# Kernel optimization log

Measured on AMD Instinct MI355X. Metric: run time of the kernel, lower is better.

The kernel has to match this reference:

```python
import jax, jax.numpy as jnp
import numpy as np

BEAM = 10; MAX_LEN = 32; PAD = 1; BOS = 2; EOS = 3
NEG = jnp.float32(-1e30)


def lstm_cell(x, h, c, Wih, Whh, bih, bhh):
    # PyTorch LSTMCell gate order: i, f, g, o
    gates = x @ Wih.T + bih + h @ Whh.T + bhh
    i, f, g, o = jnp.split(gates, 4, axis=-1)
    c2 = jax.nn.sigmoid(f) * c + jax.nn.sigmoid(i) * jnp.tanh(g)
    h2 = jax.nn.sigmoid(o) * jnp.tanh(c2)
    return h2, c2


def setup_inputs() -> dict:
    key = jax.random.key(0)
    ks = jax.random.split(key, 14)
    G, P, E, H, S = 1000, 50000, 500, 500, 32
    s = lambda k, shape: jax.random.normal(k, shape, jnp.float32) * 0.05
    return {
        "g_seq": jax.random.randint(ks[0], (S, 1), 0, G),
        "enc_emb": s(ks[1], (G, E)),
        "enc_Wih": s(ks[2], (4 * H, E)), "enc_Whh": s(ks[3], (4 * H, H)),
        "enc_bih": s(ks[4], (4 * H,)), "enc_bhh": s(ks[5], (4 * H,)),
        "dec_emb": s(ks[6], (P, E)),
        "dec_Wih": s(ks[7], (4 * H, E)), "dec_Whh": s(ks[8], (4 * H, H)),
        "dec_bih": s(ks[9], (4 * H,)), "dec_bhh": s(ks[10], (4 * H,)),
        "attn_W": s(ks[11], (H, 2 * H)),
        "out_W": s(ks[12], (P, H)),
        "out_b": s(ks[13], (P,)),
    }


def reference(g_seq, enc_emb, enc_Wih, enc_Whh, enc_bih, enc_bhh,
              dec_emb, dec_Wih, dec_Whh, dec_bih, dec_bhh,
              attn_W, out_W, out_b):
    S = g_seq.shape[0]
    H = enc_Whh.shape[1]
    P = out_W.shape[0]

    # ---- encoder: unidirectional LSTMCell over seq, batch = 1 ----
    e_seq = enc_emb[g_seq[:, 0]]  # (S, E)
    def enc_step(carry, e):
        h, c = carry
        h, c = lstm_cell(e[None, :], h, c, enc_Wih, enc_Whh, enc_bih, enc_bhh)
        return (h, c), h[0]
    h0 = jnp.zeros((1, H), jnp.float32)
    (h, c), outs = jax.lax.scan(enc_step, (h0, h0), e_seq)  # outs: (S, H)

    # expand encoder state / context to beam
    context = jnp.broadcast_to(outs[None, :, :], (BEAM, S, H))
    h = jnp.broadcast_to(h, (BEAM, H))
    c = jnp.broadcast_to(c, (BEAM, H))
    scores = jnp.zeros((BEAM,), jnp.float32)
    tokens = jnp.full((BEAM,), PAD, jnp.int32).at[0].set(BOS)
    row0 = (jnp.arange(BEAM)[:, None] == 0)  # first-step mask: only beam 0 valid

    # ---- beam-search decode loop (run full max_len; early-eos break omitted,
    #      see notes: with eos=3 it only changes output when eos tops beam 0) ----
    def dec_step(carry, t):
        h, c, scores, tokens = carry
        e = dec_emb[tokens]                                   # (BEAM, E)
        h2, c2 = lstm_cell(e, h, c, dec_Wih, dec_Whh, dec_bih, dec_bhh)
        # dot attention
        attn = jax.nn.softmax(jnp.einsum('bsh,bh->bs', context, h2), axis=1)
        wctx = jnp.einsum('bs,bsh->bh', attn, context)
        o = jnp.tanh(jnp.concatenate([h2, wctx], axis=1) @ attn_W.T)
        logp = jax.nn.log_softmax(o @ out_W.T + out_b, axis=1)  # (BEAM, P)
        # first step: only beam 0 participates (original uses workd_lk[0])
        beam_lk = jnp.where(t == 0,
                            jnp.where(row0, logp, NEG),
                            logp + scores[:, None])
        best, idx = jax.lax.top_k(beam_lk.reshape(-1), BEAM)
        prev_k = idx // P
        next_y = idx - prev_k * P
        return (h2[prev_k], c2[prev_k], best, next_y), (prev_k, next_y)

    (_, _, scores, _), (prevKs, nextYs) = jax.lax.scan(
        dec_step, (h, c, scores, tokens), jnp.arange(MAX_LEN))

    # ---- hypothesis traceback, vectorized over beams ----
    def tb_step(k, t):
        tok = nextYs[t][k]
        return prevKs[t][k], tok
    _, toks = jax.lax.scan(tb_step, jnp.arange(BEAM), jnp.arange(MAX_LEN - 1, -1, -1))
    hyps = toks[::-1].T  # (BEAM, MAX_LEN)
    return hyps
```

## Files before the change

### kernel.cpp

```cpp
#include <hip/hip_runtime.h>
#include <math.h>

#define BEAM   10
#define MAXLEN 32
#define SLEN   32
#define HD     500
#define ED     500
#define G4     2000
#define PV     50000
#define NEGF   (-1e30f)

#define OFF_X      0
#define OFF_CBUF   64000
#define OFF_GBUF   65000
#define OFF_CTX    69000
#define OFF_DH     85000
#define OFF_DC     90000
#define OFF_DG     95000
#define OFF_H2     115000
#define OFF_C2     120000
#define OFF_O      130000
#define OFF_SCD    135000
#define OFF_TOK    135020
#define OFF_PREVK  135040
#define OFF_NEXTY  135360
#define OFF_PARTD  136000
#define OFF_CAND   152000
#define OFF_LOG    160000
#define OFF_OWT    660000
#define NEED_T_BYTES ((size_t)(OFF_OWT + (size_t)HD * PV) * 4)

typedef unsigned long long u64;

__device__ __forceinline__ float sigf(float x) { return 1.f / (1.f + expf(-x)); }

__device__ __forceinline__ unsigned fkey(float f) {
    unsigned u = __float_as_uint(f);
    return (u & 0x80000000u) ? ~u : (u | 0x80000000u);
}
__device__ __forceinline__ float unfkey(unsigned k) {
    unsigned u = (k & 0x80000000u) ? (k & 0x7fffffffu) : ~k;
    return __uint_as_float(u);
}

__global__ void k_prep(const int* __restrict__ g_seq, const float* __restrict__ enc_emb,
                       const float* __restrict__ Wih, const float* __restrict__ bih,
                       const float* __restrict__ bhh, float* __restrict__ X,
                       float* __restrict__ cbuf0) {
    if (blockIdx.x == 0) {
        for (int j = threadIdx.x; j < HD; j += 256) cbuf0[j] = 0.f;
    }
    int wv = (blockIdx.x * blockDim.x + threadIdx.x) >> 6;
    int lane = threadIdx.x & 63;
    if (wv >= SLEN * G4) return;
    int t = wv / G4, r = wv - t * G4;
    const float* emb = enc_emb + (size_t)g_seq[t] * ED;
    const float* w = Wih + (size_t)r * ED;
    float acc = 0.f;
    for (int ki = 0; ki < 8; ki++) { int k = ki * 64 + lane; if (k < ED) acc += emb[k] * w[k]; }
    for (int o = 32; o; o >>= 1) acc += __shfl_down(acc, o);
    if (lane == 0) X[t * G4 + r] = acc + bih[r] + bhh[r];
}

__global__ void k_transpose4(const float* __restrict__ outW, float* __restrict__ outW4) {
    __shared__ float t_lds[64][65];
    int tid = threadIdx.x;
    int pbase = blockIdx.x * 64, kbase = blockIdx.y * 64;
    for (int e = 0; e < 16; e++) {
        int idx = e * 256 + tid; int pl = idx >> 6, kl = idx & 63;
        int pp = pbase + pl, kk = kbase + kl;
        t_lds[pl][kl] = (pp < PV && kk < HD) ? outW[(size_t)pp * HD + kk] : 0.f;
    }
    __syncthreads();
    for (int e = 0; e < 4; e++) {
        int idx = e * 256 + tid;
        int pl = idx & 63, kb = idx >> 6;
        int pp = pbase + pl;
        int kglob = kbase + kb * 4;
        if (pp < PV && kglob < HD) {
            float4 v;
            v.x = t_lds[pl][kb * 4 + 0];
            v.y = t_lds[pl][kb * 4 + 1];
            v.z = t_lds[pl][kb * 4 + 2];
            v.w = t_lds[pl][kb * 4 + 3];
            *(float4*)(outW4 + ((size_t)(kbase / 4 + kb) * PV + pp) * 4) = v;
        }
    }
}

__global__ void k_enc(const float* __restrict__ Whh, const float* __restrict__ X,
                      float* __restrict__ gbuf, float* __restrict__ cbuf,
                      float* __restrict__ context, float* __restrict__ dec_h,
                      float* __restrict__ dec_c, double* __restrict__ scores,
                      int* __restrict__ tokens, int t) {
    __shared__ float h_lds[HD];
    const float* gprev = gbuf + ((t + 1) & 1) * G4;
    float*       gcur  = gbuf + (t & 1) * G4;
    const float* cprev = cbuf + ((t + 1) & 1) * HD;
    float*       ccur  = cbuf + (t & 1) * HD;
    int tid = threadIdx.x;
    if (t > 0) {
        for (int j = tid; j < HD; j += 256) {
            float gi = gprev[j], gf = gprev[HD + j], gg = gprev[2 * HD + j], go = gprev[3 * HD + j];
            float c = sigf(gf) * cprev[j] + sigf(gi) * tanhf(gg);
            float h = sigf(go) * tanhf(c);
            h_lds[j] = h;
            if (blockIdx.x == 0) {
                ccur[j] = c;
                context[(t - 1) * HD + j] = h;
                if (t == SLEN) {
                    for (int b = 0; b < BEAM; b++) { dec_h[b * HD + j] = h; dec_c[b * HD + j] = c; }
                }
            }
        }
    } else {
        for (int j = tid; j < HD; j += 256) h_lds[j] = 0.f;
    }
    if (t == SLEN && blockIdx.x == 0 && tid == 0) {
        for (int b = 0; b < BEAM; b++) scores[b] = 0.0;
        tokens[0] = 2; for (int b = 1; b < BEAM; b++) tokens[b] = 1;
    }
    __syncthreads();
    if (t < SLEN) {
        int wv = blockIdx.x * 4 + (tid >> 6), lane = tid & 63;
        for (int r = wv; r < G4; r += 1000) {
            const float* w = Whh + (size_t)r * HD;
            float acc = 0.f;
            for (int ki = 0; ki < 8; ki++) { int k = ki * 64 + lane; if (k < HD) acc += h_lds[k] * w[k]; }
            for (int o = 32; o; o >>= 1) acc += __shfl_down(acc, o);
            if (lane == 0) gcur[r] = X[t * G4 + r] + acc;
        }
    }
}

__global__ __launch_bounds__(1024) void k_gates(
        const float* __restrict__ dec_emb, const float* __restrict__ Wih,
        const float* __restrict__ Whh, const float* __restrict__ bih,
        const float* __restrict__ bhh, const int* __restrict__ tokens,
        const float* __restrict__ h_ws, float* __restrict__ gates) {
    __shared__ float e_lds[BEAM * ED];
    __shared__ float h_lds[BEAM * HD];
    int tid = threadIdx.x;
    for (int idx = tid; idx < BEAM * ED; idx += 1024) {
        int b = idx / ED, k = idx - b * ED;
        e_lds[idx] = dec_emb[(size_t)tokens[b] * ED + k];
        h_lds[idx] = h_ws[idx];
    }
    __syncthreads();
    int wv = tid >> 6, lane = tid & 63;
    int r = blockIdx.x * 16 + wv;
    const float* wi = Wih + (size_t)r * ED;
    const float* wh = Whh + (size_t)r * HD;
    float acc[BEAM];
#pragma unroll
    for (int b = 0; b < BEAM; b++) acc[b] = 0.f;
    for (int ki = 0; ki < 8; ki++) {
        int k = ki * 64 + lane;
        if (k < ED) {
            float w = wi[k];
#pragma unroll
            for (int b = 0; b < BEAM; b++) acc[b] += w * e_lds[b * ED + k];
        }
    }
    for (int ki = 0; ki < 8; ki++) {
        int k = ki * 64 + lane;
        if (k < HD) {
            float w = wh[k];
#pragma unroll
            for (int b = 0; b < BEAM; b++) acc[b] += w * h_lds[b * HD + k];
        }
    }
#pragma unroll
    for (int b = 0; b < BEAM; b++) {
        float v = acc[b];
        for (int o = 32; o; o >>= 1) v += __shfl_down(v, o);
        acc[b] = v;
    }
    if (lane == 0) {
        float bb = bih[r] + bhh[r];
#pragma unroll
        for (int b = 0; b < BEAM; b++) gates[b * G4 + r] = acc[b] + bb;
    }
}

__global__ __launch_bounds__(256) void k_attn_oproj(
        const float* __restrict__ gates, const float* __restrict__ c_ws,
        const float* __restrict__ context, const float* __restrict__ attnW,
        float* __restrict__ h2_ws, float* __restrict__ c2_ws, float* __restrict__ o_ws) {
    __shared__ float h2_lds[BEAM * HD];
    __shared__ float wctx_lds[BEAM * HD];
    __shared__ float s_lds[BEAM * SLEN];
    __shared__ float a_lds[BEAM * SLEN];
    int tid = threadIdx.x;
    int wv = tid >> 6, lane = tid & 63;
    for (int idx = tid; idx < BEAM * HD; idx += 256) {
        int b = idx / HD, j = idx - b * HD;
        float gi = gates[b * G4 + j], gf = gates[b * G4 + HD + j];
        float gg = gates[b * G4 + 2 * HD + j], go = gates[b * G4 + 3 * HD + j];
        float c = sigf(gf) * c_ws[idx] + sigf(gi) * tanhf(gg);
        float h2 = sigf(go) * tanhf(c);
        h2_lds[idx] = h2;
        if (blockIdx.x == 0) { c2_ws[idx] = c; h2_ws[idx] = h2; }
    }
    __syncthreads();
    for (int si = 0; si < 8; ++si) {
        int s = wv + 4 * si;
        float acc[BEAM];
#pragma unroll
        for (int b = 0; b < BEAM; b++) acc[b] = 0.f;
        for (int ki = 0; ki < 8; ki++) {
            int k = ki * 64 + lane;
            if (k < HD) {
                float c = context[s * HD + k];
#pragma unroll
                for (int b = 0; b < BEAM; b++) acc[b] += c * h2_lds[b * HD + k];
            }
        }
#pragma unroll
        for (int b = 0; b < BEAM; b++) {
            float v = acc[b];
            for (int o = 32; o; o >>= 1) v += __shfl_down(v, o);
            if (lane == 0) s_lds[b * SLEN + s] = v;
        }
    }
    __syncthreads();
    if (wv == 0) {
        for (int b = 0; b < BEAM; ++b) {
            float v = (lane < SLEN) ? s_lds[b * SLEN + lane] : -INFINITY;
            float m = v;
            for (int o = 32; o; o >>= 1) m = fmaxf(m, __shfl_xor(m, o));
            float e = (lane < SLEN) ? expf(v - m) : 0.f;
            float sum = e;
            for (int o = 32; o; o >>= 1) sum += __shfl_xor(sum, o);
            if (lane < SLEN) a_lds[b * SLEN + lane] = e / sum;
        }
    }
    __syncthreads();
    {
        float w0[BEAM], w1[BEAM];
#pragma unroll
        for (int b = 0; b < BEAM; b++) { w0[b] = 0.f; w1[b] = 0.f; }
        int j0 = tid, j1 = tid + 256;
        for (int s = 0; s < SLEN; ++s) {
            float c0 = (j0 < HD) ? context[s * HD + j0] : 0.f;
            float c1 = (j1 < HD) ? context[s * HD + j1] : 0.f;
#pragma unroll
            for (int b = 0; b < BEAM; b++) {
                float a = a_lds[b * SLEN + s];
                w0[b] += a * c0; w1[b] += a * c1;
            }
        }
#pragma unroll
        for (int b = 0; b < BEAM; b++) {
            if (j0 < HD) wctx_lds[b * HD + j0] = w0[b];
            if (j1 < HD) wctx_lds[b * HD + j1] = w1[b];
        }
    }
    __syncthreads();
    int j = blockIdx.x * 4 + wv;
    const float* w = attnW + (size_t)j * 1000;
    float acc[BEAM];
#pragma unroll
    for (int b = 0; b < BEAM; b++) acc[b] = 0.f;
    for (int ki = 0; ki < 16; ki++) {
        int k = ki * 64 + lane;
        if (k < 1000) {
            float wk = w[k];
#pragma unroll
            for (int b = 0; b < BEAM; b++) {
                float h = (k < HD) ? h2_lds[b * HD + k] : wctx_lds[b * HD + k - HD];
                acc[b] += wk * h;
            }
        }
    }
#pragma unroll
    for (int b = 0; b < BEAM; b++) {
        float v = acc[b];
        for (int o = 32; o; o >>= 1) v += __shfl_down(v, o);
        acc[b] = v;
    }
    if (lane == 0) {
#pragma unroll
        for (int b = 0; b < BEAM; b++) o_ws[b * HD + j] = tanhf(acc[b]);
    }
}

__global__ __launch_bounds__(256) void k_logits4(
        const float* __restrict__ outW4, const float* __restrict__ outB,
        const float* __restrict__ o_ws, float* __restrict__ logits,
        double* __restrict__ partials) {
    __shared__ __align__(16) float4 o4[BEAM * 125];
    __shared__ float part[4][64][BEAM];
    int tid = threadIdx.x;
    for (int idx = tid; idx < BEAM * 125; idx += 256) {
        int b = idx / 125, kb = idx - b * 125;
        o4[idx] = *(const float4*)(o_ws + b * HD + kb * 4);
    }
    __syncthreads();
    int kc = tid >> 6, pl = tid & 63;
    int p = blockIdx.x * 64 + pl;
    int pc = (p < PV) ? p : (PV - 1);
    int kb0 = kc * 32, kb1 = (kc == 3) ? 125 : (kb0 + 32);
    float acc[BEAM];
#pragma unroll
    for (int b = 0; b < BEAM; b++) acc[b] = 0.f;
    const float4* wp = (const float4*)outW4;
    for (int kb = kb0; kb < kb1; ++kb) {
        float4 w = wp[(size_t)kb * PV + pc];
#pragma unroll
        for (int b = 0; b < BEAM; b++) {
            float4 o = o4[b * 125 + kb];
            acc[b] += w.x * o.x + w.y * o.y + w.z * o.z + w.w * o.w;
        }
    }
#pragma unroll
    for (int b = 0; b < BEAM; b++) part[kc][pl][b] = acc[b];
    __syncthreads();
    if (tid < 64) {
        int p2 = blockIdx.x * 64 + tid;
        bool valid = (p2 < PV);
        float ob = outB[valid ? p2 : 0];
        double es[BEAM];
#pragma unroll
        for (int b = 0; b < BEAM; b++) {
            float lg = part[0][tid][b] + part[1][tid][b] + part[2][tid][b] + part[3][tid][b] + ob;
            if (valid) logits[(size_t)b * PV + p2] = lg;
            es[b] = valid ? exp((double)lg) : 0.0;
        }
#pragma unroll
        for (int b = 0; b < BEAM; b++) {
            for (int o = 32; o; o >>= 1) es[b] += __shfl_down(es[b], o);
        }
        if (tid == 0) {
#pragma unroll
            for (int b = 0; b < BEAM; b++) partials[blockIdx.x * BEAM + b] = es[b];
        }
    }
}

__global__ void k_logits_f(const float* __restrict__ outW, const float* __restrict__ outB,
                           const float* __restrict__ o_ws, float* __restrict__ logits,
                           double* __restrict__ partials) {
    __shared__ float o_lds[BEAM * HD];
    __shared__ double ered[4][BEAM];
    int tid = threadIdx.x;
    for (int idx = tid; idx < BEAM * HD; idx += 256) o_lds[idx] = o_ws[idx];
    __syncthreads();
    int wv = tid >> 6, lane = tid & 63;
    int w = blockIdx.x * 4 + wv;
    double esum = 0.0;
    for (int pi = 0; pi < 16; pi++) {
        int p = w * 16 + pi;
        if (p >= PV) break;
        const float* wr = outW + (size_t)p * HD;
        float acc[BEAM];
#pragma unroll
        for (int b = 0; b < BEAM; b++) acc[b] = 0.f;
        for (int ki = 0; ki < 8; ki++) {
            int k = ki * 64 + lane;
            if (k < HD) {
                float x = wr[k];
#pragma unroll
                for (int b = 0; b < BEAM; b++) acc[b] += x * o_lds[b * HD + k];
            }
        }
#pragma unroll
        for (int b = 0; b < BEAM; b++)
            for (int o = 32; o; o >>= 1) acc[b] += __shfl_xor(acc[b], o);
        if (lane < BEAM) {
            float lg = 0.f;
#pragma unroll
            for (int b = 0; b < BEAM; b++) if (lane == b) lg = acc[b];
            lg += outB[p];
            logits[(size_t)lane * PV + p] = lg;
            esum += exp((double)lg);
        }
    }
    if (lane < BEAM) ered[wv][lane] = esum;
    __syncthreads();
    if (tid < BEAM) partials[blockIdx.x * BEAM + tid] =
        ered[0][tid] + ered[1][tid] + ered[2][tid] + ered[3][tid];
}

__global__ __launch_bounds__(256) void k_topk_row(const float* __restrict__ logits,
                                                  u64* __restrict__ cands) {
    const int CH = 1563;
    int r = blockIdx.x >> 5, ci = blockIdx.x & 31;
    int base = ci * CH;
    int tid = threadIdx.x;
    int wv = tid >> 6, lane = tid & 63;
    u64 key[7];
#pragma unroll
    for (int e = 0; e < 7; e++) {
        int p = base + e * 256 + tid;
        key[e] = 0ull;
        if (p < base + CH && p < PV) {
            float v = logits[(size_t)r * PV + p];
            key[e] = ((u64)fkey(v) << 32) | (unsigned)(~(unsigned)p);
        }
    }
    __shared__ u64 wred[4];
    __shared__ u64 winlds;
    for (int round = 0; round < BEAM; round++) {
        u64 mx = 0ull;
#pragma unroll
        for (int e = 0; e < 7; e++) if (key[e] > mx) mx = key[e];
        for (int o = 32; o; o >>= 1) {
            u64 other = __shfl_down(mx, o);
            if (other > mx) mx = other;
        }
        if (lane == 0) wred[wv] = mx;
        __syncthreads();
        if (tid == 0) {
            u64 wn = wred[0];
            for (int i = 1; i < 4; i++) if (wred[i] > wn) wn = wred[i];
            winlds = wn;
            cands[blockIdx.x * BEAM + round] = wn;
        }
        __syncthreads();
        u64 win = winlds;
#pragma unroll
        for (int e = 0; e < 7; e++) if (key[e] == win) key[e] = 0ull;
    }
}

__global__ __launch_bounds__(256) void k_merge(
        const double* __restrict__ partials, int npart,
        const u64* __restrict__ cands,
        double* __restrict__ scores, int* __restrict__ tokens,
        const float* __restrict__ h2_ws, const float* __restrict__ c2_ws,
        float* __restrict__ h_ws, float* __restrict__ c_ws,
        int* __restrict__ prevKs, int* __restrict__ nextYs, int t) {
    __shared__ double wredd[4];
    __shared__ double lse_lds[BEAM];
    __shared__ double sc_lds[BEAM];
    __shared__ double bwv[4];
    __shared__ unsigned bwf[4];
    __shared__ double winv_s;
    __shared__ unsigned winf_s;
    __shared__ int pk_lds[BEAM];
    __shared__ int ny_lds[BEAM];
    __shared__ double val_lds[BEAM];
    int tid = threadIdx.x;
    int wv = tid >> 6, lane = tid & 63;
    if (tid < BEAM) sc_lds[tid] = scores[tid];
    for (int b = 0; b < BEAM; b++) {
        double s = 0.0;
        for (int j = tid; j < npart; j += 256) s += partials[j * BEAM + b];
        for (int o = 32; o; o >>= 1) s += __shfl_down(s, o);
        if (lane == 0) wredd[wv] = s;
        __syncthreads();
        if (tid == 0) lse_lds[b] = log(wredd[0] + wredd[1] + wredd[2] + wredd[3]);
        __syncthreads();
    }
    double   cv[13];
    unsigned cf[13];
#pragma unroll
    for (int e = 0; e < 13; e++) {
        int c = e * 256 + tid;
        cv[e] = -1.0e308; cf[e] = 0xFFFFFFFFu;
        if (c < 3200) {
            u64 k0 = cands[c];
            if (k0) {
                int r = c / 320;
                float v = unfkey((unsigned)(k0 >> 32));
                unsigned p = ~((unsigned)k0);
                double v2;
                if (t == 0) v2 = (r == 0) ? ((double)v - lse_lds[0]) : (double)NEGF;
                else        v2 = ((double)v - lse_lds[r]) + sc_lds[r];
                cv[e] = v2;
                cf[e] = (unsigned)r * PV + p;
            }
        }
    }
    for (int round = 0; round < BEAM; round++) {
        double bv = -1.0e308; unsigned bf = 0xFFFFFFFFu;
#pragma unroll
        for (int e = 0; e < 13; e++) {
            if (cv[e] > bv || (cv[e] == bv && cf[e] < bf)) { bv = cv[e]; bf = cf[e]; }
        }
        for (int o = 32; o; o >>= 1) {
            double ov = __shfl_down(bv, o);
            unsigned of = __shfl_down(bf, o);
            if (ov > bv || (ov == bv && of < bf)) { bv = ov; bf = of; }
        }
        if (lane == 0) { bwv[wv] = bv; bwf[wv] = bf; }
        __syncthreads();
        if (tid == 0) {
            double xv = bwv[0]; unsigned xf = bwf[0];
            for (int i = 1; i < 4; i++) {
                if (bwv[i] > xv || (bwv[i] == xv && bwf[i] < xf)) { xv = bwv[i]; xf = bwf[i]; }
            }
            winv_s = xv; winf_s = xf;
            int pk = (int)(xf / PV);
            int ny = (int)(xf - (unsigned)pk * PV);
            pk_lds[round] = pk; ny_lds[round] = ny; val_lds[round] = xv;
        }
        __syncthreads();
        unsigned wff = winf_s;
#pragma unroll
        for (int e = 0; e < 13; e++) {
            if (cf[e] == wff) { cv[e] = -1.0e308; cf[e] = 0xFFFFFFFFu; }
        }
    }
    if (tid < BEAM) {
        scores[tid] = val_lds[tid];
        tokens[tid] = ny_lds[tid];
        prevKs[t * BEAM + tid] = pk_lds[tid];
        nextYs[t * BEAM + tid] = ny_lds[tid];
    }
    __syncthreads();
    for (int idx = tid; idx < BEAM * HD; idx += 256) {
        int i = idx / HD, j = idx - i * HD;
        h_ws[idx] = h2_ws[pk_lds[i] * HD + j];
        c_ws[idx] = c2_ws[pk_lds[i] * HD + j];
    }
}

__global__ void k_traceback(const int* __restrict__ prevKs, const int* __restrict__ nextYs,
                            int* __restrict__ out) {
    int k = threadIdx.x;
    if (k >= BEAM) return;
    int cur = k;
    for (int t = MAXLEN - 1; t >= 0; t--) {
        out[k * MAXLEN + t] = nextYs[t * BEAM + cur];
        cur = prevKs[t * BEAM + cur];
    }
}

extern "C" void kernel_launch(void* const* d_in, const int* in_sizes, int n_in,
                              void* d_out, int out_size, void* d_ws, size_t ws_size,
                              hipStream_t stream) {
    const int*   g_seq  = (const int*)  d_in[0];
    const float* encEmb = (const float*)d_in[1];
    const float* encWih = (const float*)d_in[2];
    const float* encWhh = (const float*)d_in[3];
    const float* encBih = (const float*)d_in[4];
    const float* encBhh = (const float*)d_in[5];
    const float* decEmb = (const float*)d_in[6];
    const float* decWih = (const float*)d_in[7];
    const float* decWhh = (const float*)d_in[8];
    const float* decBih = (const float*)d_in[9];
    const float* decBhh = (const float*)d_in[10];
    const float* attnW  = (const float*)d_in[11];
    const float* outW   = (const float*)d_in[12];
    const float* outB   = (const float*)d_in[13];

    float* ws = (float*)d_ws;
    float*  X     = ws + OFF_X;
    float*  cbuf  = ws + OFF_CBUF;
    float*  gbuf  = ws + OFF_GBUF;
    float*  ctx   = ws + OFF_CTX;
    float*  dh    = ws + OFF_DH;
    float*  dc    = ws + OFF_DC;
    float*  dg    = ws + OFF_DG;
    float*  h2    = ws + OFF_H2;
    float*  c2    = ws + OFF_C2;
    float*  o     = ws + OFF_O;
    double* sc    = (double*)(ws + OFF_SCD);
    int*    tok   = (int*)(ws + OFF_TOK);
    int*    prevK = (int*)(ws + OFF_PREVK);
    int*    nextY = (int*)(ws + OFF_NEXTY);
    double* part  = (double*)(ws + OFF_PARTD);
    u64*    cand  = (u64*)(ws + OFF_CAND);
    float*  logits = ws + OFF_LOG;
    float*  outW4  = ws + OFF_OWT;

    bool bigws = (ws_size >= NEED_T_BYTES);

    k_prep<<<16000, 256, 0, stream>>>(g_seq, encEmb, encWih, encBih, encBhh, X, cbuf);
    if (bigws) k_transpose4<<<dim3(782, 8), 256, 0, stream>>>(outW, outW4);

    for (int t = 0; t <= SLEN; t++)
        k_enc<<<250, 256, 0, stream>>>(encWhh, X, gbuf, cbuf, ctx, dh, dc, sc, tok, t);

    const int npart = 782;
    for (int t = 0; t < MAXLEN; t++) {
        k_gates<<<125, 1024, 0, stream>>>(decEmb, decWih, decWhh, decBih, decBhh, tok, dh, dg);
        k_attn_oproj<<<125, 256, 0, stream>>>(dg, dc, ctx, attnW, h2, c2, o);
        if (bigws) k_logits4<<<782, 256, 0, stream>>>(outW4, outB, o, logits, part);
        else       k_logits_f<<<782, 256, 0, stream>>>(outW, outB, o, logits, part);
        k_topk_row<<<320, 256, 0, stream>>>(logits, cand);
        k_merge<<<1, 256, 0, stream>>>(part, npart, cand, sc, tok, h2, c2, dh, dc, prevK, nextY, t);
    }
    k_traceback<<<1, 64, 0, stream>>>(prevK, nextY, (int*)d_out);
}
```

Measured before the change: 4.218 ms.

## Fuse per-strip top-k into logits kernel and merge step into gates kernel

The logits kernel now computes full 500-length dot products per vocab entry in 256-wide strips, then forms per-strip exp-sums and a per-row top-10 in shared memory. This removes the global logits buffer and the separate top-k kernel. The single-block merge is folded into the start of the gate kernel: each of the 125 blocks redundantly reruns the beam merge, then gathers h/c and embeddings by the winning indices. That drops two launches and one serialized single-block kernel per step, but every gate block repeats the merge work and the logits grid shrinks to 196 blocks.

```diff
diff --git a/kernel.cpp b/kernel.cpp
--- a/kernel.cpp
+++ b/kernel.cpp
@@ -9,6 +9,12 @@
 #define G4     2000
 #define PV     50000
 #define NEGF   (-1e30f)
+#define NEGD   (-1.0e30)
+
+#define NSTRIP 196
+#define CPR    (NSTRIP * BEAM)
+
+typedef unsigned long long u64;
 
 #define OFF_X      0
 #define OFF_CBUF   64000
@@ -19,18 +25,18 @@
 #define OFF_DG     95000
 #define OFF_H2     115000
 #define OFF_C2     120000
-#define OFF_O      130000
+#define OFF_O      125000
 #define OFF_SCD    135000
-#define OFF_TOK    135020
-#define OFF_PREVK  135040
-#define OFF_NEXTY  135360
-#define OFF_PARTD  136000
-#define OFF_CAND   152000
+#define OFF_TOK    135040
+#define OFF_PREVK  135060
+#define OFF_NEXTY  135380
+#define OFF_PARTF  136000
+#define OFF_CANDF  152000
 #define OFF_LOG    160000
+#define OFF_PARTD  160284
+#define OFF_CAND   165604
 #define OFF_OWT    660000
 #define NEED_T_BYTES ((size_t)(OFF_OWT + (size_t)HD * PV) * 4)
-
-typedef unsigned long long u64;
 
 __device__ __forceinline__ float sigf(float x) { return 1.f / (1.f + expf(-x)); }
 
@@ -133,53 +139,155 @@
     }
 }
 
-__global__ __launch_bounds__(1024) void k_gates(
-        const float* __restrict__ dec_emb, const float* __restrict__ Wih,
+struct MrgSm {
+    double lse[BEAM]; double scl[BEAM];
+    u64 rc[BEAM * BEAM];
+    double gbv[8]; unsigned gbf[8]; unsigned winf;
+    int pk[BEAM]; int ny[BEAM]; double val[BEAM];
+};
+
+__device__ __forceinline__ void do_merge(MrgSm* M, const double* __restrict__ part,
+                                         const u64* __restrict__ cand,
+                                         const double* __restrict__ sc_in,
+                                         int m, int tid) {
+    int wv = tid >> 6, lane = tid & 63;
+    if (tid < BEAM) M->scl[tid] = sc_in[tid];
+    for (int r = wv; r < BEAM; r += 8) {
+        double s = 0.0;
+        for (int i = lane; i < NSTRIP; i += 64) s += part[r * NSTRIP + i];
+        for (int o = 32; o; o >>= 1) s += __shfl_down(s, o);
+        if (lane == 0) M->lse[r] = log(s);
+    }
+    for (int r = wv; r < BEAM; r += 8) {
+        u64 kk[31];
+        int n = 0;
+        for (int i = lane; i < CPR; i += 64) kk[n++] = cand[(size_t)r * CPR + i];
+        for (; n < 31; ++n) kk[n] = 0ull;
+        for (int round = 0; round < BEAM; ++round) {
+            u64 mx = 0ull;
+#pragma unroll
+            for (int e = 0; e < 31; e++) if (kk[e] > mx) mx = kk[e];
+            for (int o = 32; o; o >>= 1) { u64 t2 = __shfl_down(mx, o); if (t2 > mx) mx = t2; }
+            u64 win = __shfl(mx, 0);
+#pragma unroll
+            for (int e = 0; e < 31; e++) if (kk[e] == win) kk[e] = 0ull;
+            if (lane == 0) M->rc[r * BEAM + round] = win;
+        }
+    }
+    __syncthreads();
+    double cv = -1.0e308; unsigned cf = 0xFFFFFFFFu;
+    if (tid < BEAM * BEAM) {
+        u64 k0 = M->rc[tid];
+        if (k0) {
+            int r2 = tid / BEAM;
+            float v = unfkey((unsigned)(k0 >> 32));
+            unsigned p = ~((unsigned)k0);
+            double v2;
+            if (m == 0) v2 = (r2 == 0) ? ((double)v - M->lse[0]) : NEGD;
+            else        v2 = ((double)v - M->lse[r2]) + M->scl[r2];
+            cv = v2; cf = (unsigned)r2 * PV + p;
+        }
+    }
+    for (int round = 0; round < BEAM; ++round) {
+        double bv = cv; unsigned bf = cf;
+        for (int o = 32; o; o >>= 1) {
+            double ov = __shfl_down(bv, o);
+            unsigned of = __shfl_down(bf, o);
+            if (ov > bv || (ov == bv && of < bf)) { bv = ov; bf = of; }
+        }
+        if (lane == 0) { M->gbv[wv] = bv; M->gbf[wv] = bf; }
+        __syncthreads();
+        if (tid == 0) {
+            double xv = M->gbv[0]; unsigned xf = M->gbf[0];
+            for (int i = 1; i < 8; i++) {
+                if (M->gbv[i] > xv || (M->gbv[i] == xv && M->gbf[i] < xf)) { xv = M->gbv[i]; xf = M->gbf[i]; }
+            }
+            M->winf = xf;
+            int pk = (int)(xf / PV);
+            int ny = (int)(xf - (unsigned)pk * PV);
+            M->pk[round] = pk; M->ny[round] = ny; M->val[round] = xv;
+        }
+        __syncthreads();
+        if (cf == M->winf) { cv = -1.0e308; cf = 0xFFFFFFFFu; }
+        __syncthreads();
+    }
+}
+
+__global__ __launch_bounds__(512) void k_gates_m(
+        const float* __restrict__ decEmb, const float* __restrict__ Wih,
         const float* __restrict__ Whh, const float* __restrict__ bih,
-        const float* __restrict__ bhh, const int* __restrict__ tokens,
-        const float* __restrict__ h_ws, float* __restrict__ gates) {
+        const float* __restrict__ bhh,
+        const double* __restrict__ part, const u64* __restrict__ cand,
+        const double* __restrict__ sc_in, double* __restrict__ sc_out,
+        const float* __restrict__ h2w, const float* __restrict__ c2w,
+        float* __restrict__ dc, const float* __restrict__ dh0,
+        int* __restrict__ prevK, int* __restrict__ nextY,
+        float* __restrict__ gates, int t) {
     __shared__ float e_lds[BEAM * ED];
     __shared__ float h_lds[BEAM * HD];
-    int tid = threadIdx.x;
-    for (int idx = tid; idx < BEAM * ED; idx += 1024) {
-        int b = idx / ED, k = idx - b * ED;
-        e_lds[idx] = dec_emb[(size_t)tokens[b] * ED + k];
-        h_lds[idx] = h_ws[idx];
-    }
-    __syncthreads();
+    __shared__ MrgSm M;
+    int tid = threadIdx.x, bid = blockIdx.x;
     int wv = tid >> 6, lane = tid & 63;
-    int r = blockIdx.x * 16 + wv;
-    const float* wi = Wih + (size_t)r * ED;
-    const float* wh = Whh + (size_t)r * HD;
-    float acc[BEAM];
-#pragma unroll
-    for (int b = 0; b < BEAM; b++) acc[b] = 0.f;
-    for (int ki = 0; ki < 8; ki++) {
-        int k = ki * 64 + lane;
-        if (k < ED) {
-            float w = wi[k];
-#pragma unroll
-            for (int b = 0; b < BEAM; b++) acc[b] += w * e_lds[b * ED + k];
-        }
-    }
-    for (int ki = 0; ki < 8; ki++) {
-        int k = ki * 64 + lane;
-        if (k < HD) {
-            float w = wh[k];
-#pragma unroll
-            for (int b = 0; b < BEAM; b++) acc[b] += w * h_lds[b * HD + k];
-        }
-    }
-#pragma unroll
-    for (int b = 0; b < BEAM; b++) {
-        float v = acc[b];
-        for (int o = 32; o; o >>= 1) v += __shfl_down(v, o);
-        acc[b] = v;
-    }
-    if (lane == 0) {
-        float bb = bih[r] + bhh[r];
-#pragma unroll
-        for (int b = 0; b < BEAM; b++) gates[b * G4 + r] = acc[b] + bb;
+
+    if (t > 0) {
+        int m = t - 1;
+        do_merge(&M, part, cand, sc_in, m, tid);
+        if (tid < BEAM && bid == 0) {
+            sc_out[tid] = M.val[tid];
+            prevK[m * BEAM + tid] = M.pk[tid];
+            nextY[m * BEAM + tid] = M.ny[tid];
+        }
+        __syncthreads();
+        for (int idx = tid; idx < BEAM * HD; idx += 512) {
+            int b = idx / HD, j = idx - b * HD;
+            h_lds[idx] = h2w[M.pk[b] * HD + j];
+            e_lds[idx] = decEmb[(size_t)M.ny[b] * ED + j];
+            if (bid == 0) dc[idx] = c2w[M.pk[b] * HD + j];
+        }
+    } else {
+        for (int idx = tid; idx < BEAM * HD; idx += 512) {
+            int b = idx / HD, j = idx - b * HD;
+            int tk = (b == 0) ? 2 : 1;
+            h_lds[idx] = dh0[idx];
+            e_lds[idx] = decEmb[(size_t)tk * ED + j];
+        }
+    }
+    __syncthreads();
+
+    for (int rr = 0; rr < 2; ++rr) {
+        int r = bid * 16 + wv * 2 + rr;
+        const float* wi = Wih + (size_t)r * ED;
+        const float* wh = Whh + (size_t)r * HD;
+        float acc[BEAM];
+#pragma unroll
+        for (int b = 0; b < BEAM; b++) acc[b] = 0.f;
+        for (int ki = 0; ki < 8; ki++) {
+            int k = ki * 64 + lane;
+            if (k < ED) {
+                float w = wi[k];
+#pragma unroll
+                for (int b = 0; b < BEAM; b++) acc[b] += w * e_lds[b * ED + k];
+            }
+        }
+        for (int ki = 0; ki < 8; ki++) {
+            int k = ki * 64 + lane;
+            if (k < HD) {
+                float w = wh[k];
+#pragma unroll
+                for (int b = 0; b < BEAM; b++) acc[b] += w * h_lds[b * HD + k];
+            }
+        }
+#pragma unroll
+        for (int b = 0; b < BEAM; b++) {
+            float v = acc[b];
+            for (int o = 32; o; o >>= 1) v += __shfl_down(v, o);
+            acc[b] = v;
+        }
+        if (lane == 0) {
+            float bb = bih[r] + bhh[r];
+#pragma unroll
+            for (int b = 0; b < BEAM; b++) gates[b * G4 + r] = acc[b] + bb;
+        }
     }
 }
 
@@ -285,56 +393,145 @@
     }
 }
 
-__global__ __launch_bounds__(256) void k_logits4(
+__global__ __launch_bounds__(256) void k_logits_topk(
         const float* __restrict__ outW4, const float* __restrict__ outB,
-        const float* __restrict__ o_ws, float* __restrict__ logits,
-        double* __restrict__ partials) {
-    __shared__ __align__(16) float4 o4[BEAM * 125];
-    __shared__ float part[4][64][BEAM];
-    int tid = threadIdx.x;
+        const float* __restrict__ o_ws, u64* __restrict__ cand,
+        double* __restrict__ part) {
+    __shared__ __align__(16) char sm[40960];
+    float4* o4 = (float4*)sm;
+    int tid = threadIdx.x, bid = blockIdx.x;
+    int wv = tid >> 6, lane = tid & 63;
     for (int idx = tid; idx < BEAM * 125; idx += 256) {
         int b = idx / 125, kb = idx - b * 125;
         o4[idx] = *(const float4*)(o_ws + b * HD + kb * 4);
     }
     __syncthreads();
-    int kc = tid >> 6, pl = tid & 63;
-    int p = blockIdx.x * 64 + pl;
-    int pc = (p < PV) ? p : (PV - 1);
-    int kb0 = kc * 32, kb1 = (kc == 3) ? 125 : (kb0 + 32);
+    int p = bid * 256 + tid;
+    bool valid = (p < PV);
+    int pc = valid ? p : (PV - 1);
+    float lg[BEAM];
+    {
+        float acc[BEAM];
+#pragma unroll
+        for (int b = 0; b < BEAM; b++) acc[b] = 0.f;
+        const float4* wp = (const float4*)outW4;
+        for (int kb = 0; kb < 125; ++kb) {
+            float4 w = wp[(size_t)kb * PV + pc];
+#pragma unroll
+            for (int b = 0; b < BEAM; b++) {
+                float4 o = o4[b * 125 + kb];
+                acc[b] += w.x * o.x + w.y * o.y + w.z * o.z + w.w * o.w;
+            }
+        }
+        float ob = outB[pc];
+#pragma unroll
+        for (int b = 0; b < BEAM; b++) lg[b] = acc[b] + ob;
+    }
+    double* pd = (double*)(sm + 20480);
+#pragma unroll
+    for (int b = 0; b < BEAM; b++) pd[b * 256 + tid] = valid ? exp((double)lg[b]) : 0.0;
+    __syncthreads();
+    for (int r = wv; r < BEAM; r += 4) {
+        double s = pd[r * 256 + lane] + pd[r * 256 + 64 + lane]
+                 + pd[r * 256 + 128 + lane] + pd[r * 256 + 192 + lane];
+        for (int o = 32; o; o >>= 1) s += __shfl_down(s, o);
+        if (lane == 0) part[r * NSTRIP + bid] = s;
+    }
+    __syncthreads();
+    u64* kl = (u64*)(sm + 20480);
+#pragma unroll
+    for (int b = 0; b < BEAM; b++)
+        kl[b * 256 + tid] = valid ? (((u64)fkey(lg[b]) << 32) | (unsigned)(~(unsigned)p)) : 0ull;
+    __syncthreads();
+    for (int r = wv; r < BEAM; r += 4) {
+        u64 kk[4];
+#pragma unroll
+        for (int j = 0; j < 4; j++) kk[j] = kl[r * 256 + j * 64 + lane];
+        for (int round = 0; round < BEAM; round++) {
+            u64 m = kk[0];
+            if (kk[1] > m) m = kk[1];
+            if (kk[2] > m) m = kk[2];
+            if (kk[3] > m) m = kk[3];
+            for (int o = 32; o; o >>= 1) {
+                u64 t2 = __shfl_down(m, o);
+                if (t2 > m) m = t2;
+            }
+            u64 win = __shfl(m, 0);
+#pragma unroll
+            for (int j = 0; j < 4; j++) if (kk[j] == win) kk[j] = 0ull;
+            if (lane == 0) cand[(size_t)r * CPR + bid * 10 + round] = win;
+        }
+    }
+}
+
+__global__ __launch_bounds__(512) void k_final(
+        const double* __restrict__ part, const u64* __restrict__ cand,
+        const double* __restrict__ sc_in,
+        int* __restrict__ prevK, int* __restrict__ nextY, int* __restrict__ out) {
+    __shared__ MrgSm M;
+    int tid = threadIdx.x;
+    do_merge(&M, part, cand, sc_in, MAXLEN - 1, tid);
+    if (tid < BEAM) {
+        prevK[(MAXLEN - 1) * BEAM + tid] = M.pk[tid];
+        nextY[(MAXLEN - 1) * BEAM + tid] = M.ny[tid];
+    }
+    __syncthreads();
+    if (tid < BEAM) {
+        int cur = tid;
+        for (int tt = MAXLEN - 1; tt >= 0; tt--) {
+            out[tid * MAXLEN + tt] = nextY[tt * BEAM + cur];
+            cur = prevK[tt * BEAM + cur];
+        }
+    }
+}
+
+__global__ __launch_bounds__(1024) void k_gates(
+        const float* __restrict__ dec_emb, const float* __restrict__ Wih,
+        const float* __restrict__ Whh, const float* __restrict__ bih,
+        const float* __restrict__ bhh, const int* __restrict__ tokens,
+        const float* __restrict__ h_ws, float* __restrict__ gates) {
+    __shared__ float e_lds[BEAM * ED];
+    __shared__ float h_lds[BEAM * HD];
+    int tid = threadIdx.x;
+    for (int idx = tid; idx < BEAM * ED; idx += 1024) {
+        int b = idx / ED, k = idx - b * ED;
+        e_lds[idx] = dec_emb[(size_t)tokens[b] * ED + k];
+        h_lds[idx] = h_ws[idx];
+    }
+    __syncthreads();
+    int wv = tid >> 6, lane = tid & 63;
+    int r = blockIdx.x * 16 + wv;
+    const float* wi = Wih + (size_t)r * ED;
+    const float* wh = Whh + (size_t)r * HD;
     float acc[BEAM];
 #pragma unroll
     for (int b = 0; b < BEAM; b++) acc[b] = 0.f;
-    const float4* wp = (const float4*)outW4;
-    for (int kb = kb0; kb < kb1; ++kb) {
-        float4 w = wp[(size_t)kb * PV + pc];
-#pragma unroll
-        for (int b = 0; b < BEAM; b++) {
-            float4 o = o4[b * 125 + kb];
-            acc[b] += w.x * o.x + w.y * o.y + w.z * o.z + w.w * o.w;
-        }
-    }
-#pragma unroll
-    for (int b = 0; b < BEAM; b++) part[kc][pl][b] = acc[b];
-    __syncthreads();
-    if (tid < 64) {
-        int p2 = blockIdx.x * 64 + tid;
-        bool valid = (p2 < PV);
-        float ob = outB[valid ? p2 : 0];
-        double es[BEAM];
-#pragma unroll
-        for (int b = 0; b < BEAM; b++) {
-            float lg = part[0][tid][b] + part[1][tid][b] + part[2][tid][b] + part[3][tid][b] + ob;
-            if (valid) logits[(size_t)b * PV + p2] = lg;
-            es[b] = valid ? exp((double)lg) : 0.0;
-        }
-#pragma unroll
-        for (int b = 0; b < BEAM; b++) {
-            for (int o = 32; o; o >>= 1) es[b] += __shfl_down(es[b], o);
-        }
-        if (tid == 0) {
-#pragma unroll
-            for (int b = 0; b < BEAM; b++) partials[blockIdx.x * BEAM + b] = es[b];
-        }
+    for (int ki = 0; ki < 8; ki++) {
+        int k = ki * 64 + lane;
+        if (k < ED) {
+            float w = wi[k];
+#pragma unroll
+            for (int b = 0; b < BEAM; b++) acc[b] += w * e_lds[b * ED + k];
+        }
+    }
+    for (int ki = 0; ki < 8; ki++) {
+        int k = ki * 64 + lane;
+        if (k < HD) {
+            float w = wh[k];
+#pragma unroll
+            for (int b = 0; b < BEAM; b++) acc[b] += w * h_lds[b * HD + k];
+        }
+    }
+#pragma unroll
+    for (int b = 0; b < BEAM; b++) {
+        float v = acc[b];
+        for (int o = 32; o; o >>= 1) v += __shfl_down(v, o);
+        acc[b] = v;
+    }
+    if (lane == 0) {
+        float bb = bih[r] + bhh[r];
+#pragma unroll
+        for (int b = 0; b < BEAM; b++) gates[b * G4 + r] = acc[b] + bb;
     }
 }
 
@@ -436,7 +633,6 @@
     __shared__ double sc_lds[BEAM];
     __shared__ double bwv[4];
     __shared__ unsigned bwf[4];
-    __shared__ double winv_s;
     __shared__ unsigned winf_s;
     __shared__ int pk_lds[BEAM];
     __shared__ int ny_lds[BEAM];
@@ -491,7 +687,7 @@
             for (int i = 1; i < 4; i++) {
                 if (bwv[i] > xv || (bwv[i] == xv && bwf[i] < xf)) { xv = bwv[i]; xf = bwf[i]; }
             }
-            winv_s = xv; winf_s = xf;
+            winf_s = xf;
             int pk = (int)(xf / PV);
             int ny = (int)(xf - (unsigned)pk * PV);
             pk_lds[round] = pk; ny_lds[round] = ny; val_lds[round] = xv;
@@ -557,14 +753,11 @@
     float*  h2    = ws + OFF_H2;
     float*  c2    = ws + OFF_C2;
     float*  o     = ws + OFF_O;
-    double* sc    = (double*)(ws + OFF_SCD);
+    double* scb   = (double*)(ws + OFF_SCD);
     int*    tok   = (int*)(ws + OFF_TOK);
     int*    prevK = (int*)(ws + OFF_PREVK);
     int*    nextY = (int*)(ws + OFF_NEXTY);
-    double* part  = (double*)(ws + OFF_PARTD);
-    u64*    cand  = (u64*)(ws + OFF_CAND);
-    float*  logits = ws + OFF_LOG;
-    float*  outW4  = ws + OFF_OWT;
+    float*  outW4 = ws + OFF_OWT;
 
     bool bigws = (ws_size >= NEED_T_BYTES);
 
@@ -572,16 +765,37 @@
     if (bigws) k_transpose4<<<dim3(782, 8), 256, 0, stream>>>(outW, outW4);
 
     for (int t = 0; t <= SLEN; t++)
-        k_enc<<<250, 256, 0, stream>>>(encWhh, X, gbuf, cbuf, ctx, dh, dc, sc, tok, t);
-
-    const int npart = 782;
-    for (int t = 0; t < MAXLEN; t++) {
-        k_gates<<<125, 1024, 0, stream>>>(decEmb, decWih, decWhh, decBih, decBhh, tok, dh, dg);
-        k_attn_oproj<<<125, 256, 0, stream>>>(dg, dc, ctx, attnW, h2, c2, o);
-        if (bigws) k_logits4<<<782, 256, 0, stream>>>(outW4, outB, o, logits, part);
-        else       k_logits_f<<<782, 256, 0, stream>>>(outW, outB, o, logits, part);
-        k_topk_row<<<320, 256, 0, stream>>>(logits, cand);
-        k_merge<<<1, 256, 0, stream>>>(part, npart, cand, sc, tok, h2, c2, dh, dc, prevK, nextY, t);
-    }
-    k_traceback<<<1, 64, 0, stream>>>(prevK, nextY, (int*)d_out);
-}
+        k_enc<<<250, 256, 0, stream>>>(encWhh, X, gbuf, cbuf, ctx, dh, dc, scb, tok, t);
+
+    if (bigws) {
+        double* part = (double*)(ws + OFF_PARTD);
+        u64*    cand = (u64*)(ws + OFF_CAND);
+        for (int t = 0; t < MAXLEN; t++) {
+            int m = t - 1;
+            const double* sin = scb + ((m & 1) ? 10 : 0);
+            double*       sout = scb + (((m + 1) & 1) ? 10 : 0);
+            if (t == 0) { sin = scb; sout = scb + 10; }
+            k_gates_m<<<125, 512, 0, stream>>>(decEmb, decWih, decWhh, decBih, decBhh,
+                                               part, cand, sin, sout,
+                                               h2, c2, dc, dh, prevK, nextY, dg, t);
+            k_attn_oproj<<<125, 256, 0, stream>>>(dg, dc, ctx, attnW, h2, c2, o);
+            k_logits_topk<<<NSTRIP, 256, 0, stream>>>(outW4, outB, o, cand, part);
+        }
+        int mf = MAXLEN - 1;
+        k_final<<<1, 512, 0, stream>>>(part, cand, scb + ((mf & 1) ? 10 : 0),
+                                       prevK, nextY, (int*)d_out);
+    } else {
+        double* part  = (double*)(ws + OFF_PARTF);
+        u64*    cand  = (u64*)(ws + OFF_CANDF);
+        float*  logits = ws + OFF_LOG;
+        const int npart = 782;
+        for (int t = 0; t < MAXLEN; t++) {
+            k_gates<<<125, 1024, 0, stream>>>(decEmb, decWih, decWhh, decBih, decBhh, tok, dh, dg);
+            k_attn_oproj<<<125, 256, 0, stream>>>(dg, dc, ctx, attnW, h2, c2, o);
+            k_logits_f<<<782, 256, 0, stream>>>(outW, outB, o, logits, part);
+            k_topk_row<<<320, 256, 0, stream>>>(logits, cand);
+            k_merge<<<1, 256, 0, stream>>>(part, npart, cand, scb, tok, h2, c2, dh, dc, prevK, nextY, t);
+        }
+        k_traceback<<<1, 64, 0, stream>>>(prevK, nextY, (int*)d_out);
+    }
+}
```

After: 5.726 ms. 35.8% more time.
